# Kernel optimization log

Hardware: AMD Instinct MI355X
Metric: run time of the kernel (lower is better)

Reference implementation:

```python
import jax, jax.numpy as jnp
import numpy as np

N, C, L = 64, 3, 4096
K, S = 128, 64  # num_shapelets, shapelets_size


def setup_inputs() -> dict:
    key = jax.random.key(0)
    kx, ks = jax.random.split(key)
    x = jax.random.normal(kx, (N, C, L), dtype=jnp.float32)
    shapelets = jax.random.normal(ks, (C, K, S), dtype=jnp.float32)
    return {"x": x, "shapelets": shapelets}


def _min_euclid(x, shapelets):
    # x: (N, C, L); shapelets: (C, K, S)
    # Torch does unfold -> cdist -> min over windows -> min over channels.
    # We compute ||x_w - s||^2 = ||x_w||^2 + ||s||^2 - 2<x_w, s> with sliding
    # dot products via grouped 1-D conv (avoids materializing the unfold).
    C_, K_, S_ = shapelets.shape
    n = x.shape[0]
    filt = shapelets.reshape(C_ * K_, 1, S_)  # OIW, grouped by channel
    dots = jax.lax.conv_general_dilated(
        x, filt, window_strides=(1,), padding="VALID",
        dimension_numbers=("NCW", "OIW", "NCW"),
        feature_group_count=C_)                      # (N, C*K, W)
    ones = jnp.ones((C_, 1, S_), x.dtype)
    x2 = jax.lax.conv_general_dilated(
        x * x, ones, window_strides=(1,), padding="VALID",
        dimension_numbers=("NCW", "OIW", "NCW"),
        feature_group_count=C_)                      # (N, C, W) sliding ||x_w||^2
    W_ = dots.shape[-1]
    dots = dots.reshape(n, C_, K_, W_)               # (N, C, K, W)
    s2 = jnp.sum(shapelets * shapelets, axis=-1)     # (C, K)
    d2 = x2[:, :, None, :] + s2[None, :, :, None] - 2.0 * dots
    d = jnp.sqrt(jnp.maximum(d2, 0.0))               # Euclidean distance (N,C,K,W)
    d = jnp.min(d, axis=3)                           # min over windows -> (N, C, K)
    d = jnp.min(d, axis=1)                           # min over channels -> (N, K)
    return d[:, None, :]                             # (N, 1, K)


def reference(x, shapelets):
    return _min_euclid(x, shapelets)
```

## Files before the change

kernel.cpp:

```cpp
#include <hip/hip_runtime.h>
#include <hip/hip_bf16.h>

#define NN 64
#define CC 3
#define LL 4096
#define SS 64
#define KK 128
#define WW 4033
#define BLKN 8

typedef __attribute__((ext_vector_type(8))) short v8s;
typedef __attribute__((ext_vector_type(4))) float v4f;

#define WS_CNT_OFF 32768
#define WS_HS2_OFF 33024
#define WS_SHB_OFF 34560
#define WS_HX2_OFF 131072

__device__ __forceinline__ unsigned bf16_rne(float f) {
    unsigned u = __float_as_uint(f);
    return (u + 0x7FFFu + ((u >> 16) & 1u)) >> 16;
}

__global__ __launch_bounds__(256) void me_prep(
        const float* __restrict__ x,
        const float* __restrict__ shp,
        unsigned* __restrict__ d2g,
        unsigned* __restrict__ cnt,
        float* __restrict__ hs2g,
        uint4* __restrict__ shb,
        float* __restrict__ hx2g) {
    const int b = blockIdx.x, t = threadIdx.x;
    if (b < NN * CC) {
        const int n = b / 3, c = b - n * 3;
        __shared__ float P[LL];
        __shared__ float wtot[4];
        const int lane = t & 63, wave = t >> 6;
        const float* xc = x + ((size_t)n * CC + c) * LL;
        const int base = t * 16;
        float q[16];
        {
            float4 A0 = *(const float4*)(xc + base);
            float4 A1 = *(const float4*)(xc + base + 4);
            float4 A2 = *(const float4*)(xc + base + 8);
            float4 A3 = *(const float4*)(xc + base + 12);
            q[0]=A0.x; q[1]=A0.y; q[2]=A0.z;  q[3]=A0.w;
            q[4]=A1.x; q[5]=A1.y; q[6]=A1.z;  q[7]=A1.w;
            q[8]=A2.x; q[9]=A2.y; q[10]=A2.z; q[11]=A2.w;
            q[12]=A3.x;q[13]=A3.y;q[14]=A3.z; q[15]=A3.w;
        }
        float run = 0.f;
        #pragma unroll
        for (int i = 0; i < 16; ++i) { run += q[i] * q[i]; q[i] = run; }
        float sc = run;
        #pragma unroll
        for (int d = 1; d < 64; d <<= 1) {
            float u = __shfl_up(sc, d, 64);
            if (lane >= d) sc += u;
        }
        if (lane == 63) wtot[wave] = sc;
        __syncthreads();
        float excl = sc - run;
        for (int w2 = 0; w2 < wave; ++w2) excl += wtot[w2];
        #pragma unroll
        for (int i = 0; i < 16; ++i) q[i] += excl;
        *(float4*)(P + base)      = make_float4(q[0], q[1], q[2], q[3]);
        *(float4*)(P + base + 4)  = make_float4(q[4], q[5], q[6], q[7]);
        *(float4*)(P + base + 8)  = make_float4(q[8], q[9], q[10], q[11]);
        *(float4*)(P + base + 12) = make_float4(q[12], q[13], q[14], q[15]);
        __syncthreads();
        float* dst = hx2g + ((size_t)n * CC + c) * LL;
        #pragma unroll
        for (int i = 0; i < 16; ++i) {
            int w = base + i;
            float o = -1e30f;
            if (w < WW) {
                float I1 = P[w + 63];
                float I0 = (w > 0) ? P[w - 1] : 0.f;
                o = -0.5f * (I1 - I0);
            }
            dst[w] = o;
        }
    } else {
        int tid = (b - NN * CC) * 256 + t;
        if (tid < NN * KK) d2g[tid] = 0x7F800000u;
        if (tid < NN) cnt[tid] = 0u;
        if (tid < CC * KK) {
            const float* r = shp + tid * SS;
            float a = 0.f;
            #pragma unroll 8
            for (int s = 0; s < SS; ++s) a += r[s] * r[s];
            hs2g[tid] = -0.5f * a;
        }
        if (tid < CC * 1024) {
            int c   = tid >> 10;
            int r   = tid & 1023;
            int nt  = r >> 7;
            int scb = (r >> 6) & 1;
            int l   = r & 63;
            int row  = nt * 16 + (l & 15);
            int koff = scb * 32 + (l >> 4) * 8;
            const float* s = shp + ((size_t)(c * KK + row)) * SS + koff;
            float4 f0 = *(const float4*)s;
            float4 f1 = *(const float4*)(s + 4);
            uint4 o;
            o.x = (bf16_rne(f0.y) << 16) | bf16_rne(f0.x);
            o.y = (bf16_rne(f0.w) << 16) | bf16_rne(f0.z);
            o.z = (bf16_rne(f1.y) << 16) | bf16_rne(f1.x);
            o.w = (bf16_rne(f1.w) << 16) | bf16_rne(f1.z);
            shb[tid] = o;
        }
    }
}

__global__ __launch_bounds__(256, 2) void me_main(
        const float* __restrict__ x,
        const ushort* __restrict__ shb_g,
        const float* __restrict__ hs2g,
        const float* __restrict__ hx2g,
        unsigned* __restrict__ d2g,
        unsigned* __restrict__ cnt,
        float* __restrict__ out) {

    __shared__ __align__(16) ushort shb[CC * 8192];
    __shared__ __align__(8) ushort xs2[2][2][CC][320];
    __shared__ unsigned red[KK];
    __shared__ int lastflag;

    const int b    = blockIdx.x;
    const int n    = b >> 3;
    const int tg   = b & 7;
    const int t    = threadIdx.x;
    const int lane = t & 63, wave = t >> 6;
    const int quad = lane >> 4, col = lane & 15;
    const int wbase = wave * 64;

    if (t < KK) red[t] = 0x7F800000u;

    {
        typedef __attribute__((address_space(1))) const uint4 gu4;
        typedef __attribute__((address_space(3))) uint4 lu4;
        const uint4* gbase = (const uint4*)shb_g;
        #pragma unroll
        for (int it = 0; it < 12; ++it) {
            const uint4* gp = gbase + it * 256 + t;
            uint4* lp = (uint4*)shb + (it * 256 + wave * 64);
            __builtin_amdgcn_global_load_lds((gu4*)gp, (lu4*)lp, 16, 0, 0);
        }
    }

    float hsv[CC][8];
    #pragma unroll
    for (int c = 0; c < CC; ++c)
        #pragma unroll
        for (int nt = 0; nt < 8; ++nt)
            hsv[c][nt] = hs2g[c * KK + nt * 16 + col];

    const float* xb   = x + (size_t)n * (CC * LL);
    const float* hx2b = hx2g + (size_t)n * (CC * LL);

    float rmax[8];
    #pragma unroll
    for (int nt = 0; nt < 8; ++nt) rmax[nt] = -3.4e38f;

    for (int it = 0; it < 2; ++it) {
        const int buf = it;
        const int w0  = tg * 512 + it * 256;

        if (t < 240) {
            int c = t / 80, q = t - c * 80;
            int idx = q * 4, gi = w0 + idx;
            float4 v;
            if (gi + 3 < LL) v = *(const float4*)(xb + c * LL + gi);
            else {
                v.x = (gi     < LL) ? xb[c * LL + gi]     : 0.f;
                v.y = (gi + 1 < LL) ? xb[c * LL + gi + 1] : 0.f;
                v.z = (gi + 2 < LL) ? xb[c * LL + gi + 2] : 0.f;
                v.w = (gi + 3 < LL) ? xb[c * LL + gi + 3] : 0.f;
            }
            unsigned h0 = bf16_rne(v.x), h1 = bf16_rne(v.y);
            unsigned h2 = bf16_rne(v.z), h3 = bf16_rne(v.w);
            uint2 p0; p0.x = h0 | (h1 << 16); p0.y = h2 | (h3 << 16);
            *(uint2*)&xs2[buf][0][c][idx] = p0;
            if (idx > 0) xs2[buf][1][c][idx - 1] = (ushort)h0;
            *(uint*)&xs2[buf][1][c][idx] = h1 | (h2 << 16);
            xs2[buf][1][c][idx + 2] = (ushort)h3;
        }
        __syncthreads();

        #pragma unroll
        for (int c = 0; c < CC; ++c) {
            const float* hp = hx2b + c * LL + w0 + wbase + quad * 4;
            v4f hxv[4];
            #pragma unroll
            for (int mt = 0; mt < 4; ++mt) hxv[mt] = *(const v4f*)(hp + mt * 16);
            v8s af[4][2];
            #pragma unroll
            for (int mt = 0; mt < 4; ++mt)
                #pragma unroll
                for (int sc = 0; sc < 2; ++sc) {
                    int e0 = wbase + mt * 16 + col + sc * 32 + quad * 8;
                    int p  = col & 1;
                    const uint* ap = (const uint*)&xs2[buf][p][c][e0 - p];
                    union { v8s v; uint u[4]; } au;
                    au.u[0] = ap[0]; au.u[1] = ap[1];
                    au.u[2] = ap[2]; au.u[3] = ap[3];
                    af[mt][sc] = au.v;
                }
            #pragma unroll
            for (int g = 0; g < 2; ++g) {
                v4f acc[4][4];
                #pragma unroll
                for (int nt2 = 0; nt2 < 4; ++nt2) {
                    float h = hsv[c][g * 4 + nt2];
                    v4f a = {h, h, h, h};
                    #pragma unroll
                    for (int mt = 0; mt < 4; ++mt) acc[nt2][mt] = a;
                }
                #pragma unroll
                for (int sc = 0; sc < 2; ++sc)
                    #pragma unroll
                    for (int nt2 = 0; nt2 < 4; ++nt2) {
                        int nt = g * 4 + nt2;
                        v8s bfr = *(const v8s*)(shb + (((c * 8 + nt) * 2 + sc) * 64 + lane) * 8);
                        #pragma unroll
                        for (int mt = 0; mt < 4; ++mt)
                            acc[nt2][mt] = __builtin_amdgcn_mfma_f32_16x16x32_bf16(
                                af[mt][sc], bfr, acc[nt2][mt], 0, 0, 0);
                    }
                #pragma unroll
                for (int nt2 = 0; nt2 < 4; ++nt2) {
                    float m = -3.4e38f;
                    #pragma unroll
                    for (int mt = 0; mt < 4; ++mt) {
                        v4f a = acc[nt2][mt];
                        #pragma unroll
                        for (int r = 0; r < 4; ++r)
                            m = fmaxf(m, a[r] + hxv[mt][r]);
                    }
                    rmax[g * 4 + nt2] = fmaxf(rmax[g * 4 + nt2], m);
                }
            }
        }
    }

    #pragma unroll
    for (int nt = 0; nt < 8; ++nt) {
        float v = rmax[nt];
        v = fmaxf(v, __shfl_xor(v, 16, 64));
        v = fmaxf(v, __shfl_xor(v, 32, 64));
        rmax[nt] = v;
    }
    if (quad == 0) {
        #pragma unroll
        for (int nt = 0; nt < 8; ++nt) {
            float d2 = fmaxf(-2.f * rmax[nt], 0.f);
            atomicMin(&red[nt * 16 + col], __float_as_uint(d2));
        }
    }
    __syncthreads();
    if (t < KK) atomicMin(&d2g[n * KK + t], red[t]);

    __syncthreads();
    if (t == 0) {
        unsigned old = atomicAdd(&cnt[n], 1u);
        lastflag = (old == BLKN - 1) ? 1 : 0;
    }
    __syncthreads();
    if (lastflag && t < KK) {
        unsigned bits = atomicMin(&d2g[n * KK + t], 0x7F800000u);
        out[n * KK + t] = sqrtf(__uint_as_float(bits));
    }
}

extern "C" void kernel_launch(void* const* d_in, const int* in_sizes, int n_in,
                              void* d_out, int out_size, void* d_ws, size_t ws_size,
                              hipStream_t stream) {
    const float* x   = (const float*)d_in[0];
    const float* shp = (const float*)d_in[1];
    unsigned* d2g  = (unsigned*)d_ws;
    unsigned* cnt  = (unsigned*)((char*)d_ws + WS_CNT_OFF);
    float*    hs2g = (float*)((char*)d_ws + WS_HS2_OFF);
    uint4*    shb  = (uint4*)((char*)d_ws + WS_SHB_OFF);
    float*    hx2g = (float*)((char*)d_ws + WS_HX2_OFF);
    float* out = (float*)d_out;

    hipLaunchKernelGGL(me_prep, dim3(NN * CC + 32), dim3(256), 0, stream,
                       x, shp, d2g, cnt, hs2g, shb, hx2g);
    hipLaunchKernelGGL(me_main, dim3(NN * BLKN), dim3(256), 0, stream,
                       x, (const ushort*)shb, hs2g, hx2g, d2g, cnt, out);
}
```

Baseline: 76.92 us.

## Stage full 512-window tile once and widen per-wave M tile to 128

The main kernel now loads the block's whole 512-window x slice (plus halo) into LDS in one pass with a single barrier, replacing the two-iteration loop. Each wave now covers 128 windows with 8 M-tiles and 2 N-tiles per group, so each shapelet B fragment read from LDS is reused across more MFMAs. The prep kernel is cut to 128 blocks, each prefix-summing two (n,c) rows, so its grid fits in one wave of CUs. The trade-off is higher register pressure from 8x2 accumulators and 8 A fragments, which may reduce occupancy or cause spills.

```diff
diff --git a/kernel.cpp b/kernel.cpp
--- a/kernel.cpp
+++ b/kernel.cpp
@@ -31,58 +31,62 @@
         uint4* __restrict__ shb,
         float* __restrict__ hx2g) {
     const int b = blockIdx.x, t = threadIdx.x;
-    if (b < NN * CC) {
-        const int n = b / 3, c = b - n * 3;
+    if (b < 96) {
         __shared__ float P[LL];
         __shared__ float wtot[4];
         const int lane = t & 63, wave = t >> 6;
-        const float* xc = x + ((size_t)n * CC + c) * LL;
         const int base = t * 16;
-        float q[16];
-        {
-            float4 A0 = *(const float4*)(xc + base);
-            float4 A1 = *(const float4*)(xc + base + 4);
-            float4 A2 = *(const float4*)(xc + base + 8);
-            float4 A3 = *(const float4*)(xc + base + 12);
-            q[0]=A0.x; q[1]=A0.y; q[2]=A0.z;  q[3]=A0.w;
-            q[4]=A1.x; q[5]=A1.y; q[6]=A1.z;  q[7]=A1.w;
-            q[8]=A2.x; q[9]=A2.y; q[10]=A2.z; q[11]=A2.w;
-            q[12]=A3.x;q[13]=A3.y;q[14]=A3.z; q[15]=A3.w;
-        }
-        float run = 0.f;
-        #pragma unroll
-        for (int i = 0; i < 16; ++i) { run += q[i] * q[i]; q[i] = run; }
-        float sc = run;
-        #pragma unroll
-        for (int d = 1; d < 64; d <<= 1) {
-            float u = __shfl_up(sc, d, 64);
-            if (lane >= d) sc += u;
-        }
-        if (lane == 63) wtot[wave] = sc;
-        __syncthreads();
-        float excl = sc - run;
-        for (int w2 = 0; w2 < wave; ++w2) excl += wtot[w2];
-        #pragma unroll
-        for (int i = 0; i < 16; ++i) q[i] += excl;
-        *(float4*)(P + base)      = make_float4(q[0], q[1], q[2], q[3]);
-        *(float4*)(P + base + 4)  = make_float4(q[4], q[5], q[6], q[7]);
-        *(float4*)(P + base + 8)  = make_float4(q[8], q[9], q[10], q[11]);
-        *(float4*)(P + base + 12) = make_float4(q[12], q[13], q[14], q[15]);
-        __syncthreads();
-        float* dst = hx2g + ((size_t)n * CC + c) * LL;
-        #pragma unroll
-        for (int i = 0; i < 16; ++i) {
-            int w = base + i;
-            float o = -1e30f;
-            if (w < WW) {
-                float I1 = P[w + 63];
-                float I0 = (w > 0) ? P[w - 1] : 0.f;
-                o = -0.5f * (I1 - I0);
-            }
-            dst[w] = o;
+        for (int s2 = 0; s2 < 2; ++s2) {
+            const int id = 2 * b + s2;
+            const int n = id / 3, c = id - n * 3;
+            if (s2) __syncthreads();
+            const float* xc = x + ((size_t)n * CC + c) * LL;
+            float q[16];
+            {
+                float4 A0 = *(const float4*)(xc + base);
+                float4 A1 = *(const float4*)(xc + base + 4);
+                float4 A2 = *(const float4*)(xc + base + 8);
+                float4 A3 = *(const float4*)(xc + base + 12);
+                q[0]=A0.x; q[1]=A0.y; q[2]=A0.z;  q[3]=A0.w;
+                q[4]=A1.x; q[5]=A1.y; q[6]=A1.z;  q[7]=A1.w;
+                q[8]=A2.x; q[9]=A2.y; q[10]=A2.z; q[11]=A2.w;
+                q[12]=A3.x;q[13]=A3.y;q[14]=A3.z; q[15]=A3.w;
+            }
+            float run = 0.f;
+            #pragma unroll
+            for (int i = 0; i < 16; ++i) { run += q[i] * q[i]; q[i] = run; }
+            float sc = run;
+            #pragma unroll
+            for (int d = 1; d < 64; d <<= 1) {
+                float u = __shfl_up(sc, d, 64);
+                if (lane >= d) sc += u;
+            }
+            if (lane == 63) wtot[wave] = sc;
+            __syncthreads();
+            float excl = sc - run;
+            for (int w2 = 0; w2 < wave; ++w2) excl += wtot[w2];
+            #pragma unroll
+            for (int i = 0; i < 16; ++i) q[i] += excl;
+            *(float4*)(P + base)      = make_float4(q[0], q[1], q[2], q[3]);
+            *(float4*)(P + base + 4)  = make_float4(q[4], q[5], q[6], q[7]);
+            *(float4*)(P + base + 8)  = make_float4(q[8], q[9], q[10], q[11]);
+            *(float4*)(P + base + 12) = make_float4(q[12], q[13], q[14], q[15]);
+            __syncthreads();
+            float* dst = hx2g + ((size_t)n * CC + c) * LL;
+            #pragma unroll
+            for (int i = 0; i < 16; ++i) {
+                int w = base + i;
+                float o = -1e30f;
+                if (w < WW) {
+                    float I1 = P[w + 63];
+                    float I0 = (w > 0) ? P[w - 1] : 0.f;
+                    o = -0.5f * (I1 - I0);
+                }
+                dst[w] = o;
+            }
         }
     } else {
-        int tid = (b - NN * CC) * 256 + t;
+        int tid = (b - 96) * 256 + t;
         if (tid < NN * KK) d2g[tid] = 0x7F800000u;
         if (tid < NN) cnt[tid] = 0u;
         if (tid < CC * KK) {
@@ -123,17 +127,18 @@
         float* __restrict__ out) {
 
     __shared__ __align__(16) ushort shb[CC * 8192];
-    __shared__ __align__(8) ushort xs2[2][2][CC][320];
+    __shared__ __align__(8) ushort xs2[2][CC][640];
     __shared__ unsigned red[KK];
     __shared__ int lastflag;
 
     const int b    = blockIdx.x;
     const int n    = b >> 3;
     const int tg   = b & 7;
+    const int w0   = tg * 512;
     const int t    = threadIdx.x;
     const int lane = t & 63, wave = t >> 6;
     const int quad = lane >> 4, col = lane & 15;
-    const int wbase = wave * 64;
+    const int wbase = wave * 128;
 
     if (t < KK) red[t] = 0x7F800000u;
 
@@ -159,17 +164,12 @@
     const float* xb   = x + (size_t)n * (CC * LL);
     const float* hx2b = hx2g + (size_t)n * (CC * LL);
 
-    float rmax[8];
-    #pragma unroll
-    for (int nt = 0; nt < 8; ++nt) rmax[nt] = -3.4e38f;
-
+    #pragma unroll
     for (int it = 0; it < 2; ++it) {
-        const int buf = it;
-        const int w0  = tg * 512 + it * 256;
-
-        if (t < 240) {
-            int c = t / 80, q = t - c * 80;
-            int idx = q * 4, gi = w0 + idx;
+        int e = t + it * 256;
+        if (e < 432) {
+            int c = e / 144, qd = e - c * 144;
+            int idx = qd * 4, gi = w0 + idx;
             float4 v;
             if (gi + 3 < LL) v = *(const float4*)(xb + c * LL + gi);
             else {
@@ -181,65 +181,69 @@
             unsigned h0 = bf16_rne(v.x), h1 = bf16_rne(v.y);
             unsigned h2 = bf16_rne(v.z), h3 = bf16_rne(v.w);
             uint2 p0; p0.x = h0 | (h1 << 16); p0.y = h2 | (h3 << 16);
-            *(uint2*)&xs2[buf][0][c][idx] = p0;
-            if (idx > 0) xs2[buf][1][c][idx - 1] = (ushort)h0;
-            *(uint*)&xs2[buf][1][c][idx] = h1 | (h2 << 16);
-            xs2[buf][1][c][idx + 2] = (ushort)h3;
-        }
-        __syncthreads();
-
-        #pragma unroll
-        for (int c = 0; c < CC; ++c) {
-            const float* hp = hx2b + c * LL + w0 + wbase + quad * 4;
-            v4f hxv[4];
-            #pragma unroll
-            for (int mt = 0; mt < 4; ++mt) hxv[mt] = *(const v4f*)(hp + mt * 16);
-            v8s af[4][2];
-            #pragma unroll
-            for (int mt = 0; mt < 4; ++mt)
+            *(uint2*)&xs2[0][c][idx] = p0;
+            if (idx > 0) xs2[1][c][idx - 1] = (ushort)h0;
+            *(uint*)&xs2[1][c][idx] = h1 | (h2 << 16);
+            xs2[1][c][idx + 2] = (ushort)h3;
+        }
+    }
+    __syncthreads();
+
+    float rmax[8];
+    #pragma unroll
+    for (int nt = 0; nt < 8; ++nt) rmax[nt] = -3.4e38f;
+
+    #pragma unroll
+    for (int c = 0; c < CC; ++c) {
+        const float* hp = hx2b + c * LL + w0 + wbase + quad * 4;
+        v4f hxv[8];
+        #pragma unroll
+        for (int mt = 0; mt < 8; ++mt) hxv[mt] = *(const v4f*)(hp + mt * 16);
+        v8s af[8][2];
+        #pragma unroll
+        for (int mt = 0; mt < 8; ++mt)
+            #pragma unroll
+            for (int sc = 0; sc < 2; ++sc) {
+                int e0 = wbase + mt * 16 + col + sc * 32 + quad * 8;
+                int p  = col & 1;
+                const uint* ap = (const uint*)&xs2[p][c][e0 - p];
+                union { v8s v; uint u[4]; } au;
+                au.u[0] = ap[0]; au.u[1] = ap[1];
+                au.u[2] = ap[2]; au.u[3] = ap[3];
+                af[mt][sc] = au.v;
+            }
+        #pragma unroll
+        for (int g = 0; g < 4; ++g) {
+            v4f acc[2][8];
+            #pragma unroll
+            for (int nt2 = 0; nt2 < 2; ++nt2) {
+                float h = hsv[c][g * 2 + nt2];
+                v4f a = {h, h, h, h};
                 #pragma unroll
-                for (int sc = 0; sc < 2; ++sc) {
-                    int e0 = wbase + mt * 16 + col + sc * 32 + quad * 8;
-                    int p  = col & 1;
-                    const uint* ap = (const uint*)&xs2[buf][p][c][e0 - p];
-                    union { v8s v; uint u[4]; } au;
-                    au.u[0] = ap[0]; au.u[1] = ap[1];
-                    au.u[2] = ap[2]; au.u[3] = ap[3];
-                    af[mt][sc] = au.v;
+                for (int mt = 0; mt < 8; ++mt) acc[nt2][mt] = a;
+            }
+            #pragma unroll
+            for (int sc = 0; sc < 2; ++sc)
+                #pragma unroll
+                for (int nt2 = 0; nt2 < 2; ++nt2) {
+                    int nt = g * 2 + nt2;
+                    v8s bfr = *(const v8s*)(shb + (((c * 8 + nt) * 2 + sc) * 64 + lane) * 8);
+                    #pragma unroll
+                    for (int mt = 0; mt < 8; ++mt)
+                        acc[nt2][mt] = __builtin_amdgcn_mfma_f32_16x16x32_bf16(
+                            af[mt][sc], bfr, acc[nt2][mt], 0, 0, 0);
                 }
             #pragma unroll
-            for (int g = 0; g < 2; ++g) {
-                v4f acc[4][4];
+            for (int nt2 = 0; nt2 < 2; ++nt2) {
+                float m = -3.4e38f;
                 #pragma unroll
-                for (int nt2 = 0; nt2 < 4; ++nt2) {
-                    float h = hsv[c][g * 4 + nt2];
-                    v4f a = {h, h, h, h};
+                for (int mt = 0; mt < 8; ++mt) {
+                    v4f a = acc[nt2][mt];
                     #pragma unroll
-                    for (int mt = 0; mt < 4; ++mt) acc[nt2][mt] = a;
+                    for (int r = 0; r < 4; ++r)
+                        m = fmaxf(m, a[r] + hxv[mt][r]);
                 }
-                #pragma unroll
-                for (int sc = 0; sc < 2; ++sc)
-                    #pragma unroll
-                    for (int nt2 = 0; nt2 < 4; ++nt2) {
-                        int nt = g * 4 + nt2;
-                        v8s bfr = *(const v8s*)(shb + (((c * 8 + nt) * 2 + sc) * 64 + lane) * 8);
-                        #pragma unroll
-                        for (int mt = 0; mt < 4; ++mt)
-                            acc[nt2][mt] = __builtin_amdgcn_mfma_f32_16x16x32_bf16(
-                                af[mt][sc], bfr, acc[nt2][mt], 0, 0, 0);
-                    }
-                #pragma unroll
-                for (int nt2 = 0; nt2 < 4; ++nt2) {
-                    float m = -3.4e38f;
-                    #pragma unroll
-                    for (int mt = 0; mt < 4; ++mt) {
-                        v4f a = acc[nt2][mt];
-                        #pragma unroll
-                        for (int r = 0; r < 4; ++r)
-                            m = fmaxf(m, a[r] + hxv[mt][r]);
-                    }
-                    rmax[g * 4 + nt2] = fmaxf(rmax[g * 4 + nt2], m);
-                }
+                rmax[g * 2 + nt2] = fmaxf(rmax[g * 2 + nt2], m);
             }
         }
     }
@@ -285,7 +289,7 @@
     float*    hx2g = (float*)((char*)d_ws + WS_HX2_OFF);
     float* out = (float*)d_out;
 
-    hipLaunchKernelGGL(me_prep, dim3(NN * CC + 32), dim3(256), 0, stream,
+    hipLaunchKernelGGL(me_prep, dim3(128), dim3(256), 0, stream,
                        x, shp, d2g, cnt, hs2g, shb, hx2g);
     hipLaunchKernelGGL(me_main, dim3(NN * BLKN), dim3(256), 0, stream,
                        x, (const ushort*)shb, hs2g, hx2g, d2g, cnt, out);
```

New measurement: 77.23 us. Within noise of the previous version (+0.4%).
